# Performance work log

Hardware: AMD Instinct MI355X
Metric: run time of the kernel (lower is better)

## Reference

```python
import jax, jax.numpy as jnp
import numpy as np

B, S, D, H = 2, 2048, 2048, 16
DK = D // H  # 128


def _rope(x, cos, sin):
    # x: [B,S,H,DK]; pairs (x0,x1),(x2,x3),... rotated as complex numbers
    xr = x[..., 0::2]  # [B,S,H,DK/2]
    xi = x[..., 1::2]
    yr = xr * cos - xi * sin
    yi = xr * sin + xi * cos
    y = jnp.stack([yr, yi], axis=-1)  # [B,S,H,DK/2,2]
    return y.reshape(x.shape)


def setup_inputs() -> dict:
    key = jax.random.key(0)
    ks = jax.random.split(key, 12)
    sc = 1.0 / np.sqrt(D)
    q = jax.random.normal(ks[0], (B, S, D), jnp.float32)
    k = jax.random.normal(ks[1], (B, S, D), jnp.float32)
    v = jax.random.normal(ks[2], (B, S, D), jnp.float32)
    mask = jnp.tril(jnp.ones((S, S), jnp.int32))[None, None]  # causal [1,1,S,S]
    # standard RoPE angles: pos * theta^(-2i/dk)
    theta = 10000.0 ** (-jnp.arange(0, DK, 2, dtype=jnp.float32) / DK)  # [DK/2]
    freqs_angles = jnp.arange(S, dtype=jnp.float32)[:, None] * theta[None, :]  # [S,DK/2]
    wq = jax.random.normal(ks[3], (D, D), jnp.float32) * sc
    bq = jax.random.normal(ks[4], (D,), jnp.float32) * 0.01
    wk = jax.random.normal(ks[5], (D, D), jnp.float32) * sc
    bk = jax.random.normal(ks[6], (D,), jnp.float32) * 0.01
    wv = jax.random.normal(ks[7], (D, D), jnp.float32) * sc
    bv = jax.random.normal(ks[8], (D,), jnp.float32) * 0.01
    wo = jax.random.normal(ks[9], (D, D), jnp.float32) * sc
    bo = jax.random.normal(ks[10], (D,), jnp.float32) * 0.01
    return dict(q=q, k=k, v=v, mask=mask, freqs_angles=freqs_angles,
                wq=wq, bq=bq, wk=wk, bk=bk, wv=wv, bv=bv, wo=wo, bo=bo)


def reference(q, k, v, mask, freqs_angles, wq, bq, wk, bk, wv, bv, wo, bo):
    query = q @ wq.T + bq
    key_ = k @ wk.T + bk
    value = v @ wv.T + bv
    query = query.reshape(B, S, H, DK)
    key_ = key_.reshape(B, S, H, DK)
    value = value.reshape(B, S, H, DK).transpose(0, 2, 1, 3)  # [B,H,S,DK]
    cos = jnp.cos(freqs_angles)[None, :, None, :]  # [1,S,1,DK/2]
    sin = jnp.sin(freqs_angles)[None, :, None, :]
    query = _rope(query, cos, sin).transpose(0, 2, 1, 3)  # [B,H,S,DK]
    key_ = _rope(key_, cos, sin).transpose(0, 2, 1, 3)
    scores = jnp.einsum('bhqd,bhkd->bhqk', query, key_) / jnp.sqrt(jnp.float32(DK))
    scores = jnp.where(mask == 0, jnp.float32(-1e9), scores)
    attn = jax.nn.softmax(scores, axis=-1)  # dropout p=0.0 -> identity
    x = jnp.einsum('bhqk,bhkd->bhqd', attn, value)
    x = x.transpose(0, 2, 1, 3).reshape(B, S, D)
    return x @ wo.T + bo
```

## Files before the change

### kernel.cpp

```cpp
#include <hip/hip_runtime.h>
#include <hip/hip_bf16.h>

#define BB 2
#define SS 2048
#define DD 2048
#define HH 16
#define DKK 128
#define MM (BB*SS)

typedef unsigned short u16;
typedef short bf16x8 __attribute__((ext_vector_type(8)));
typedef unsigned short u16x8 __attribute__((ext_vector_type(8)));
typedef float f32x4 __attribute__((ext_vector_type(4)));

static __device__ __forceinline__ f32x4 mfma_bf16(bf16x8 a, bf16x8 b, f32x4 c) {
  return __builtin_amdgcn_mfma_f32_16x16x32_bf16(a, b, c, 0, 0, 0);
}

static __device__ __forceinline__ u16 f2b(float f) {
  unsigned int u = __float_as_uint(f);
  u = (u + 0x7FFFu + ((u >> 16) & 1u)) >> 16;
  return (u16)u;
}

static __device__ __forceinline__ u16 f2bq(float f) {
  unsigned int r;
  asm("v_cvt_pk_bf16_f32 %0, %1, %2" : "=v"(r) : "v"(f), "v"(f));
  return (u16)r;
}

static __device__ __forceinline__ void gl16(const u16* g, u16* l) {
  __builtin_amdgcn_global_load_lds(
      (const __attribute__((address_space(1))) unsigned int*)(const void*)g,
      (__attribute__((address_space(3))) unsigned int*)(void*)l, 16, 0, 0);
}

#define BARRIER() asm volatile("s_barrier" ::: "memory")

struct F2BArgs { const float* src[7]; u16* dst[7]; };
__global__ __launch_bounds__(256) void k_f2bf_all(F2BArgs a) {
  int bid = blockIdx.x;
  int buf, local;
  if (bid < 12288) { buf = bid >> 12; local = bid & 4095; }
  else { int t = bid - 12288; buf = 3 + (t >> 11); local = t & 2047; }
  const int i = (local * 256 + threadIdx.x) * 8;
  const float* in = a.src[buf];
  float4 v0 = *reinterpret_cast<const float4*>(in + i);
  float4 v1 = *reinterpret_cast<const float4*>(in + i + 4);
  u16x8 o;
  o[0]=f2b(v0.x); o[1]=f2b(v0.y); o[2]=f2b(v0.z); o[3]=f2b(v0.w);
  o[4]=f2b(v1.x); o[5]=f2b(v1.y); o[6]=f2b(v1.z); o[7]=f2b(v1.w);
  *reinterpret_cast<u16x8*>(a.dst[buf] + i) = o;
}

__global__ void k_cs(const float* __restrict__ fa, float* __restrict__ cs, int n) {
  int t = blockIdx.x * blockDim.x + threadIdx.x;
  if (t >= n) return;
  float a = fa[t];
  cs[2*t]   = cosf(a);
  cs[2*t+1] = sinf(a);
}

struct GemmJob { const u16* A; const u16* W; const float* bias; void* out; int mode; };
struct GemmArgs { GemmJob job[3]; };

__global__ __launch_bounds__(512, 2) void k_gemm256(GemmArgs ga, const float* __restrict__ cs) {
  const GemmJob J = ga.job[blockIdx.z];
  const u16* __restrict__ A = J.A;
  const u16* __restrict__ W = J.W;
  const int mode = J.mode;
  const int K = DD, N = DD;
  const int KT = K / 64;

  __shared__ __align__(16) u16 sA[2][256 * 64];
  __shared__ __align__(16) u16 sB[2][256 * 64];

  const int tid = threadIdx.x;
  const int l  = tid & 63;
  const int w  = tid >> 6;
  const int wm = w >> 2;
  const int wn = w & 3;
  const int bm = blockIdx.x * 256, bn = blockIdx.y * 256;
  const int lr = l & 15;
  const int lg = l >> 4;
  const int rx = (lr & 7) * 8;

  const int srcx = ((l & 7) * 8) ^ ((l >> 3) * 8);
  const size_t rowA = (size_t)(bm + w*16 + (l >> 3)) * K + srcx;
  const size_t rowB = (size_t)(bn + w*16 + (l >> 3)) * K + srcx;
  const int ldsrow = (w * 16) * 64;

  f32x4 acc[8][4];
#pragma unroll
  for (int m = 0; m < 8; m++)
#pragma unroll
    for (int n = 0; n < 4; n++)
#pragma unroll
      for (int j = 0; j < 4; j++) acc[m][n][j] = 0.0f;

  auto stA = [&](int kt, int h) {
    const u16* g = A + rowA + (size_t)h * 128 * K + kt * 64;
    u16* d = &sA[kt & 1][h * 128 * 64 + ldsrow];
    gl16(g, d);
    gl16(g + (size_t)8 * K, d + 8 * 64);
  };
  auto stB = [&](int kt, int h) {
    const u16* g = W + rowB + (size_t)h * 128 * K + kt * 64;
    u16* d = &sB[kt & 1][h * 128 * 64 + ldsrow];
    gl16(g, d);
    gl16(g + (size_t)8 * K, d + 8 * 64);
  };

  stB(0, 0); stB(0, 1); stA(0, 0); stA(0, 1);
  stB(1, 0); stB(1, 1);
  asm volatile("s_waitcnt vmcnt(4)" ::: "memory");
  BARRIER();

#pragma unroll 1
  for (int t = 0; t < KT; t++) {
    const u16* a_ = sA[t & 1];
    const u16* b_ = sB[t & 1];
    bf16x8 a03[4][2], a47[4][2], b01[2][2], b23[2][2];

#pragma unroll
    for (int m = 0; m < 4; m++)
#pragma unroll
      for (int kk = 0; kk < 2; kk++)
        a03[m][kk] = *reinterpret_cast<const bf16x8*>(
            a_ + (wm*128 + m*16 + lr) * 64 + ((kk*32 + lg*8) ^ rx));
#pragma unroll
    for (int n = 0; n < 2; n++)
#pragma unroll
      for (int kk = 0; kk < 2; kk++)
        b01[n][kk] = *reinterpret_cast<const bf16x8*>(
            b_ + (wn*64 + n*16 + lr) * 64 + ((kk*32 + lg*8) ^ rx));
    if (t + 1 < KT) stA(t + 1, 0);
    BARRIER();
    __builtin_amdgcn_s_setprio(1);
#pragma unroll
    for (int kk = 0; kk < 2; kk++)
#pragma unroll
      for (int m = 0; m < 4; m++)
#pragma unroll
        for (int n = 0; n < 2; n++)
          acc[m][n] = mfma_bf16(a03[m][kk], b01[n][kk], acc[m][n]);
    __builtin_amdgcn_s_setprio(0);
    BARRIER();

#pragma unroll
    for (int n = 0; n < 2; n++)
#pragma unroll
      for (int kk = 0; kk < 2; kk++)
        b23[n][kk] = *reinterpret_cast<const bf16x8*>(
            b_ + (wn*64 + (n + 2)*16 + lr) * 64 + ((kk*32 + lg*8) ^ rx));
    if (t + 1 < KT) stA(t + 1, 1);
    BARRIER();
    __builtin_amdgcn_s_setprio(1);
#pragma unroll
    for (int kk = 0; kk < 2; kk++)
#pragma unroll
      for (int m = 0; m < 4; m++)
#pragma unroll
        for (int n = 0; n < 2; n++)
          acc[m][n + 2] = mfma_bf16(a03[m][kk], b23[n][kk], acc[m][n + 2]);
    __builtin_amdgcn_s_setprio(0);
    BARRIER();

#pragma unroll
    for (int m = 0; m < 4; m++)
#pragma unroll
      for (int kk = 0; kk < 2; kk++)
        a47[m][kk] = *reinterpret_cast<const bf16x8*>(
            a_ + (wm*128 + (m + 4)*16 + lr) * 64 + ((kk*32 + lg*8) ^ rx));
    if (t + 2 < KT) stB(t + 2, 0);
    BARRIER();
    __builtin_amdgcn_s_setprio(1);
#pragma unroll
    for (int kk = 0; kk < 2; kk++)
#pragma unroll
      for (int m = 0; m < 4; m++)
#pragma unroll
        for (int n = 0; n < 2; n++)
          acc[m + 4][n] = mfma_bf16(a47[m][kk], b01[n][kk], acc[m + 4][n]);
    __builtin_amdgcn_s_setprio(0);
    BARRIER();

    if (t + 2 < KT) stB(t + 2, 1);
    BARRIER();
    __builtin_amdgcn_s_setprio(1);
#pragma unroll
    for (int kk = 0; kk < 2; kk++)
#pragma unroll
      for (int m = 0; m < 4; m++)
#pragma unroll
        for (int n = 0; n < 2; n++)
          acc[m + 4][n + 2] = mfma_bf16(a47[m][kk], b23[n][kk], acc[m + 4][n + 2]);
    __builtin_amdgcn_s_setprio(0);
    if (t + 2 < KT) {
      asm volatile("s_waitcnt vmcnt(4)" ::: "memory");
    } else {
      asm volatile("s_waitcnt vmcnt(0)" ::: "memory");
    }
    BARRIER();
  }

  float bv[4];
#pragma unroll
  for (int n = 0; n < 4; n++) bv[n] = J.bias[bn + wn*64 + n*16 + lr];
#pragma unroll
  for (int m = 0; m < 8; m++) {
#pragma unroll
    for (int n = 0; n < 4; n++) {
      const int col = bn + wn*64 + n*16 + lr;
#pragma unroll
      for (int r = 0; r < 4; r++) {
        const int row = bm + wm*128 + m*16 + lg*4 + r;
        float v = acc[m][n][r] + bv[n];
        if (mode & 1) {
          const int s  = row & (SS - 1);
          const int dk = col & (DKK - 1);
          const int p  = dk >> 1;
          const float2 csv = *reinterpret_cast<const float2*>(cs + (size_t)(s*64 + p)*2);
          const float other = __shfl_xor(v, 1);
          const float sgn = (dk & 1) ? csv.y : -csv.y;
          v = v * csv.x + other * sgn;
          if (mode == 3) v *= 0.12751744f;
        }
        if (mode == 2) {
          reinterpret_cast<float*>(J.out)[(size_t)row * N + col] = v;
        } else {
          reinterpret_cast<u16*>(J.out)[(size_t)row * N + col] = f2b(v);
        }
      }
    }
  }
}

__global__ __launch_bounds__(256) void k_gemm3(GemmArgs ga, const float* __restrict__ cs) {
  const GemmJob J = ga.job[blockIdx.z];
  const u16* __restrict__ A = J.A;
  const u16* __restrict__ W = J.W;
  const int mode = J.mode;
  const int K = DD, N = DD;

  __shared__ __align__(16) u16 sA[128 * 64];
  __shared__ __align__(16) u16 sB[128 * 64];
  const int tid = threadIdx.x;
  const int l  = tid & 63;
  const int w  = tid >> 6;
  const int wr = w >> 1, wc = w & 1;
  const int bm = blockIdx.x * 128, bn = blockIdx.y * 128;
  const int lr = l & 15;
  const int lg = l >> 4;

  f32x4 acc[4][4];
#pragma unroll
  for (int mi = 0; mi < 4; mi++)
#pragma unroll
    for (int ni = 0; ni < 4; ni++)
#pragma unroll
      for (int j = 0; j < 4; j++) acc[mi][ni][j] = 0.0f;

  const int srcx = ((l & 7) * 8) ^ ((l >> 3) * 8);
  const u16* gAl = A + (size_t)(bm + w*32 + (l >> 3)) * K + srcx;
  const u16* gBl = W + (size_t)(bn + w*32 + (l >> 3)) * K + srcx;

  const int rx = (lr & 7) * 8;

  for (int k0 = 0; k0 < K; k0 += 64) {
    __syncthreads();
#pragma unroll
    for (int i = 0; i < 4; i++) gl16(gAl + (size_t)i*8*K + k0, sA + (w*32 + i*8) * 64);
#pragma unroll
    for (int i = 0; i < 4; i++) gl16(gBl + (size_t)i*8*K + k0, sB + (w*32 + i*8) * 64);
    __syncthreads();

#pragma unroll
    for (int kk = 0; kk < 2; kk++) {
      bf16x8 af[4], bfv[4];
#pragma unroll
      for (int i = 0; i < 4; i++)
        af[i]  = *reinterpret_cast<const bf16x8*>(
            sA + (wr*64 + i*16 + lr) * 64 + ((kk*32 + lg*8) ^ rx));
#pragma unroll
      for (int i = 0; i < 4; i++)
        bfv[i] = *reinterpret_cast<const bf16x8*>(
            sB + (wc*64 + i*16 + lr) * 64 + ((kk*32 + lg*8) ^ rx));
#pragma unroll
      for (int mi = 0; mi < 4; mi++)
#pragma unroll
        for (int ni = 0; ni < 4; ni++)
          acc[mi][ni] = mfma_bf16(af[mi], bfv[ni], acc[mi][ni]);
    }
  }

#pragma unroll
  for (int mi = 0; mi < 4; mi++) {
#pragma unroll
    for (int ni = 0; ni < 4; ni++) {
      const int col = bn + wc*64 + ni*16 + lr;
      const float bv = J.bias[col];
#pragma unroll
      for (int r = 0; r < 4; r++) {
        const int row = bm + wr*64 + mi*16 + lg*4 + r;
        float v = acc[mi][ni][r] + bv;
        if (mode & 1) {
          const int s  = row & (SS - 1);
          const int dk = col & (DKK - 1);
          const int p  = dk >> 1;
          const float2 csv = *reinterpret_cast<const float2*>(cs + (size_t)(s*64 + p)*2);
          const float other = __shfl_xor(v, 1);
          const float sgn = (dk & 1) ? csv.y : -csv.y;
          v = v * csv.x + other * sgn;
          if (mode == 3) v *= 0.12751744f;
        }
        if (mode == 2) {
          reinterpret_cast<float*>(J.out)[(size_t)row * N + col] = v;
        } else {
          reinterpret_cast<u16*>(J.out)[(size_t)row * N + col] = f2b(v);
        }
      }
    }
  }
}

__global__ __launch_bounds__(256, 1) void k_attn(const u16* __restrict__ Qp,
                                                 const u16* __restrict__ Kp,
                                                 const u16* __restrict__ Vp,
                                                 u16* __restrict__ Op) {
  const int bid = blockIdx.x;
  const int qt = 15 - (bid >> 5);
  const int bh = bid & 31;
  const int h  = bh & 15;
  const int b  = bh >> 4;
  const int tid = threadIdx.x;
  const int l  = tid & 63, w = tid >> 6;
  const int lr = l & 15, lg = l >> 4;

  __shared__ __align__(16) u16 Klds[2 * 128 * 128];
  __shared__ __align__(16) u16 VT[128 * 128];
  __shared__ __align__(16) u16 PL[4][32][136];

  int koff[8];
#pragma unroll
  for (int i = 0; i < 8; i++) {
    const int row = w*32 + i*4 + (l >> 4);
    koff[i] = row * DD + (((l & 15) * 8) ^ ((row & 7) * 8));
  }
  const u16* kbase = Kp + (size_t)b * SS * DD + h * DKK;

  const int k0v = (tid >> 4) * 8;
  const int d0  = (tid & 15) * 8;
  const u16* vbase = Vp + (size_t)b * SS * DD + h * DKK + (size_t)k0v * DD + d0;

  uint4 vr[8];

  auto stageK = [&](int nk, int bufq) {
    const u16* kb = kbase + (size_t)nk * (128 * DD);
    u16* dst = Klds + bufq * 16384 + (w * 32) * 128;
#pragma unroll
    for (int i = 0; i < 8; i++) gl16(kb + koff[i], dst + i * 512);
  };
  auto prefV = [&](int nk) {
    const u16* vb = vbase + (size_t)nk * (128 * DD);
#pragma unroll
    for (int c = 0; c < 8; c++) vr[c] = *reinterpret_cast<const uint4*>(vb + c * DD);
  };

  int cur = 0;
  stageK(0, 0);
  prefV(0);

  bf16x8 qf[2][4];
#pragma unroll
  for (int mt = 0; mt < 2; mt++) {
    const size_t qrow = (size_t)(b*SS + qt*128 + w*32 + mt*16 + lr) * DD + h*DKK;
#pragma unroll
    for (int kk = 0; kk < 4; kk++)
      qf[mt][kk] = *reinterpret_cast<const bf16x8*>(Qp + qrow + kk*32 + lg*8);
  }

  float m[2][4], lsum[2][4];
  f32x4 oacc[2][8];
#pragma unroll
  for (int mt = 0; mt < 2; mt++)
#pragma unroll
    for (int r = 0; r < 4; r++) { m[mt][r] = -INFINITY; lsum[mt][r] = 0.0f; }
#pragma unroll
  for (int mt = 0; mt < 2; mt++)
#pragma unroll
    for (int dt = 0; dt < 8; dt++)
#pragma unroll
      for (int jj = 0; jj < 4; jj++) oacc[mt][dt][jj] = 0.0f;

#pragma unroll 1
  for (int kv = 0; kv <= qt; kv++) {
    __syncthreads();
#pragma unroll
    for (int dj = 0; dj < 8; dj++) {
      const int row = d0 + dj;
      const int col = k0v ^ (((row ^ (row >> 3)) & 15) * 8);
      u16x8 pk;
#pragma unroll
      for (int j = 0; j < 8; j++) pk[j] = reinterpret_cast<const u16*>(&vr[j])[dj];
      *reinterpret_cast<u16x8*>(VT + row * 128 + col) = pk;
    }
    __syncthreads();

    const bool hasnext = (kv < qt);
    if (hasnext) {
      prefV(kv + 1);
      stageK(kv + 1, cur ^ 1);
    }

    f32x4 sa[2][8];
#pragma unroll
    for (int mt = 0; mt < 2; mt++)
#pragma unroll
      for (int kt = 0; kt < 8; kt++)
#pragma unroll
        for (int jj = 0; jj < 4; jj++) sa[mt][kt][jj] = 0.0f;
    const u16* kl = Klds + cur * 16384;
    __builtin_amdgcn_s_setprio(1);
#pragma unroll
    for (int kk = 0; kk < 4; kk++) {
#pragma unroll
      for (int kt = 0; kt < 8; kt++) {
        const int row = kt*16 + lr;
        const bf16x8 kf = *reinterpret_cast<const bf16x8*>(
            kl + row * 128 + ((kk*32 + lg*8) ^ ((row & 7) * 8)));
#pragma unroll
        for (int mt = 0; mt < 2; mt++)
          sa[mt][kt] = mfma_bf16(qf[mt][kk], kf, sa[mt][kt]);
      }
    }
    __builtin_amdgcn_s_setprio(0);

    if (kv == qt) {
#pragma unroll
      for (int kt = 0; kt < 8; kt++) {
        const int key = kv*128 + kt*16 + lr;
#pragma unroll
        for (int mt = 0; mt < 2; mt++)
#pragma unroll
          for (int r = 0; r < 4; r++) {
            const int qv = qt*128 + w*32 + mt*16 + lg*4 + r;
            if (key > qv) sa[mt][kt][r] = -1e9f;
          }
      }
    }

    float pm[2][4];
#pragma unroll
    for (int mt = 0; mt < 2; mt++)
#pragma unroll
      for (int r = 0; r < 4; r++) {
        float t0 = fmaxf(fmaxf(sa[mt][0][r], sa[mt][1][r]), fmaxf(sa[mt][2][r], sa[mt][3][r]));
        float t1 = fmaxf(fmaxf(sa[mt][4][r], sa[mt][5][r]), fmaxf(sa[mt][6][r], sa[mt][7][r]));
        pm[mt][r] = fmaxf(t0, t1);
      }
    bool ok = true;
#pragma unroll
    for (int mt = 0; mt < 2; mt++)
#pragma unroll
      for (int r = 0; r < 4; r++) ok = ok && (pm[mt][r] <= m[mt][r] + 8.0f);
    if (!__all(ok)) {
#pragma unroll
      for (int mt = 0; mt < 2; mt++)
#pragma unroll
        for (int r = 0; r < 4; r++) {
          float t = pm[mt][r];
#pragma unroll
          for (int d = 1; d < 16; d <<= 1) t = fmaxf(t, __shfl_xor(t, d));
          const float mnew = fmaxf(m[mt][r], t);
          const float corr = exp2f(m[mt][r] - mnew);
          lsum[mt][r] *= corr;
#pragma unroll
          for (int dt = 0; dt < 8; dt++) oacc[mt][dt][r] *= corr;
          m[mt][r] = mnew;
        }
    }

#pragma unroll
    for (int mt = 0; mt < 2; mt++)
#pragma unroll
      for (int r = 0; r < 4; r++) {
        float rs = 0.0f;
#pragma unroll
        for (int kt = 0; kt < 8; kt++) {
          const float e = exp2f(sa[mt][kt][r] - m[mt][r]);
          rs += e;
          PL[w][mt*16 + lg*4 + r][kt*16 + lr] = f2bq(e);
        }
        lsum[mt][r] += rs;
      }

    __builtin_amdgcn_s_setprio(1);
#pragma unroll
    for (int kk2 = 0; kk2 < 4; kk2++) {
      bf16x8 pa[2];
#pragma unroll
      for (int mt = 0; mt < 2; mt++)
        pa[mt] = *reinterpret_cast<const bf16x8*>(&PL[w][mt*16 + lr][kk2*32 + lg*8]);
#pragma unroll
      for (int dt = 0; dt < 8; dt++) {
        const int row = dt*16 + lr;
        const bf16x8 vb = *reinterpret_cast<const bf16x8*>(
            VT + row * 128 + ((kk2*32 + lg*8) ^ (((row ^ (row >> 3)) & 15) * 8)));
#pragma unroll
        for (int mt = 0; mt < 2; mt++)
          oacc[mt][dt] = mfma_bf16(pa[mt], vb, oacc[mt][dt]);
      }
    }
    __builtin_amdgcn_s_setprio(0);

    if (hasnext) cur ^= 1;
  }

  float inv[2][4];
#pragma unroll
  for (int mt = 0; mt < 2; mt++)
#pragma unroll
    for (int r = 0; r < 4; r++) {
      float t = lsum[mt][r];
#pragma unroll
      for (int d = 1; d < 16; d <<= 1) t += __shfl_xor(t, d);
      inv[mt][r] = 1.0f / t;
    }
#pragma unroll
  for (int mt = 0; mt < 2; mt++)
#pragma unroll
    for (int dt = 0; dt < 8; dt++)
#pragma unroll
      for (int r = 0; r < 4; r++) {
        const size_t row = (size_t)(b*SS + qt*128 + w*32 + mt*16 + lg*4 + r);
        Op[row * DD + h*DKK + dt*16 + lr] = f2bq(oacc[mt][dt][r] * inv[mt][r]);
      }
}

extern "C" void kernel_launch(void* const* d_in, const int* in_sizes, int n_in,
                              void* d_out, int out_size, void* d_ws, size_t ws_size,
                              hipStream_t stream) {
  const float* q  = (const float*)d_in[0];
  const float* k  = (const float*)d_in[1];
  const float* v  = (const float*)d_in[2];
  const float* fa = (const float*)d_in[4];
  const float* wq = (const float*)d_in[5];
  const float* bq = (const float*)d_in[6];
  const float* wk = (const float*)d_in[7];
  const float* bk = (const float*)d_in[8];
  const float* wv = (const float*)d_in[9];
  const float* bv = (const float*)d_in[10];
  const float* wo = (const float*)d_in[11];
  const float* bo = (const float*)d_in[12];

  float* cs = (float*)d_ws;
  u16* bf = (u16*)((char*)d_ws + (size_t)262144 * sizeof(float));
  const size_t NX = (size_t)MM * DD;
  const size_t NW = (size_t)DD * DD;
  u16* q_bf  = bf;
  u16* k_bf  = q_bf + NX;
  u16* v_bf  = k_bf + NX;
  u16* wq_bf = v_bf + NX;
  u16* wk_bf = wq_bf + NW;
  u16* wv_bf = wk_bf + NW;
  u16* wo_bf = wv_bf + NW;
  u16* Qp    = wo_bf + NW;
  u16* Kp    = Qp + NX;
  u16* Vp    = Kp + NX;
  u16* Ao    = Vp + NX;

  F2BArgs fa7;
  fa7.src[0] = q;  fa7.dst[0] = q_bf;
  fa7.src[1] = k;  fa7.dst[1] = k_bf;
  fa7.src[2] = v;  fa7.dst[2] = v_bf;
  fa7.src[3] = wq; fa7.dst[3] = wq_bf;
  fa7.src[4] = wk; fa7.dst[4] = wk_bf;
  fa7.src[5] = wv; fa7.dst[5] = wv_bf;
  fa7.src[6] = wo; fa7.dst[6] = wo_bf;
  k_f2bf_all<<<dim3(20480), 256, 0, stream>>>(fa7);
  k_cs<<<dim3(131072/256), 256, 0, stream>>>(fa, cs, 131072);

  GemmArgs gq;
  gq.job[0] = GemmJob{ q_bf, wq_bf, bq, (void*)Qp, 3 };
  gq.job[1] = GemmJob{ k_bf, wk_bf, bk, (void*)Kp, 1 };
  gq.job[2] = GemmJob{ v_bf, wv_bf, bv, (void*)Vp, 0 };
  k_gemm256<<<dim3(MM/256, DD/256, 3), 512, 0, stream>>>(gq, cs);

  k_attn<<<dim3(512), 256, 0, stream>>>(Qp, Kp, Vp, Ao);

  GemmArgs go;
  go.job[0] = GemmJob{ Ao, wo_bf, bo, d_out, 2 };
  go.job[1] = go.job[0];
  go.job[2] = go.job[0];
  k_gemm3<<<dim3(MM/128, DD/128, 1), 256, 0, stream>>>(go, cs);
}
```

Measured before the change: 348.3 us.

## Reorder GEMM tile load quarters to prefetch A further ahead, pin schedule

```diff
diff --git a/kernel.cpp b/kernel.cpp
--- a/kernel.cpp
+++ b/kernel.cpp
@@ -86,9 +86,7 @@
   const int rx = (lr & 7) * 8;
 
   const int srcx = ((l & 7) * 8) ^ ((l >> 3) * 8);
-  const size_t rowA = (size_t)(bm + w*16 + (l >> 3)) * K + srcx;
-  const size_t rowB = (size_t)(bn + w*16 + (l >> 3)) * K + srcx;
-  const int ldsrow = (w * 16) * 64;
+  const int l3 = l >> 3;
 
   f32x4 acc[8][4];
 #pragma unroll
@@ -98,22 +96,24 @@
 #pragma unroll
       for (int j = 0; j < 4; j++) acc[m][n][j] = 0.0f;
 
-  auto stA = [&](int kt, int h) {
-    const u16* g = A + rowA + (size_t)h * 128 * K + kt * 64;
-    u16* d = &sA[kt & 1][h * 128 * 64 + ldsrow];
+  auto stA2 = [&](int kt, int q) {
+    const int R0 = (w & 3) * 16 + (w >> 2) * 128 + q * 64;
+    const u16* g = A + (size_t)(bm + R0 + l3) * K + srcx + kt * 64;
+    u16* d = &sA[kt & 1][R0 * 64];
     gl16(g, d);
     gl16(g + (size_t)8 * K, d + 8 * 64);
   };
-  auto stB = [&](int kt, int h) {
-    const u16* g = W + rowB + (size_t)h * 128 * K + kt * 64;
-    u16* d = &sB[kt & 1][h * 128 * 64 + ldsrow];
+  auto stB2 = [&](int kt, int q) {
+    const int R0 = (w >> 1) * 64 + (w & 1) * 16 + q * 32;
+    const u16* g = W + (size_t)(bn + R0 + l3) * K + srcx + kt * 64;
+    u16* d = &sB[kt & 1][R0 * 64];
     gl16(g, d);
     gl16(g + (size_t)8 * K, d + 8 * 64);
   };
 
-  stB(0, 0); stB(0, 1); stA(0, 0); stA(0, 1);
-  stB(1, 0); stB(1, 1);
-  asm volatile("s_waitcnt vmcnt(4)" ::: "memory");
+  stA2(0, 0); stA2(0, 1); stB2(0, 0); stB2(0, 1);
+  stA2(1, 0); stB2(1, 0); stB2(1, 1);
+  asm volatile("s_waitcnt vmcnt(6)" ::: "memory");
   BARRIER();
 
 #pragma unroll 1
@@ -134,8 +134,9 @@
       for (int kk = 0; kk < 2; kk++)
         b01[n][kk] = *reinterpret_cast<const bf16x8*>(
             b_ + (wn*64 + n*16 + lr) * 64 + ((kk*32 + lg*8) ^ rx));
-    if (t + 1 < KT) stA(t + 1, 0);
-    BARRIER();
+    if (t + 1 < KT) stA2(t + 1, 1);
+    BARRIER();
+    __builtin_amdgcn_sched_barrier(0);
     __builtin_amdgcn_s_setprio(1);
 #pragma unroll
     for (int kk = 0; kk < 2; kk++)
@@ -145,6 +146,7 @@
         for (int n = 0; n < 2; n++)
           acc[m][n] = mfma_bf16(a03[m][kk], b01[n][kk], acc[m][n]);
     __builtin_amdgcn_s_setprio(0);
+    __builtin_amdgcn_sched_barrier(0);
     BARRIER();
 
 #pragma unroll
@@ -153,8 +155,9 @@
       for (int kk = 0; kk < 2; kk++)
         b23[n][kk] = *reinterpret_cast<const bf16x8*>(
             b_ + (wn*64 + (n + 2)*16 + lr) * 64 + ((kk*32 + lg*8) ^ rx));
-    if (t + 1 < KT) stA(t + 1, 1);
-    BARRIER();
+    if (t + 2 < KT) stA2(t + 2, 0);
+    BARRIER();
+    __builtin_amdgcn_sched_barrier(0);
     __builtin_amdgcn_s_setprio(1);
 #pragma unroll
     for (int kk = 0; kk < 2; kk++)
@@ -164,6 +167,7 @@
         for (int n = 0; n < 2; n++)
           acc[m][n + 2] = mfma_bf16(a03[m][kk], b23[n][kk], acc[m][n + 2]);
     __builtin_amdgcn_s_setprio(0);
+    __builtin_amdgcn_sched_barrier(0);
     BARRIER();
 
 #pragma unroll
@@ -172,8 +176,9 @@
       for (int kk = 0; kk < 2; kk++)
         a47[m][kk] = *reinterpret_cast<const bf16x8*>(
             a_ + (wm*128 + (m + 4)*16 + lr) * 64 + ((kk*32 + lg*8) ^ rx));
-    if (t + 2 < KT) stB(t + 2, 0);
-    BARRIER();
+    if (t + 2 < KT) stB2(t + 2, 0);
+    BARRIER();
+    __builtin_amdgcn_sched_barrier(0);
     __builtin_amdgcn_s_setprio(1);
 #pragma unroll
     for (int kk = 0; kk < 2; kk++)
@@ -183,10 +188,12 @@
         for (int n = 0; n < 2; n++)
           acc[m + 4][n] = mfma_bf16(a47[m][kk], b01[n][kk], acc[m + 4][n]);
     __builtin_amdgcn_s_setprio(0);
-    BARRIER();
-
-    if (t + 2 < KT) stB(t + 2, 1);
-    BARRIER();
+    __builtin_amdgcn_sched_barrier(0);
+    BARRIER();
+
+    if (t + 2 < KT) stB2(t + 2, 1);
+    BARRIER();
+    __builtin_amdgcn_sched_barrier(0);
     __builtin_amdgcn_s_setprio(1);
 #pragma unroll
     for (int kk = 0; kk < 2; kk++)
@@ -196,8 +203,9 @@
         for (int n = 0; n < 2; n++)
           acc[m + 4][n + 2] = mfma_bf16(a47[m][kk], b23[n][kk], acc[m + 4][n + 2]);
     __builtin_amdgcn_s_setprio(0);
-    if (t + 2 < KT) {
-      asm volatile("s_waitcnt vmcnt(4)" ::: "memory");
+    __builtin_amdgcn_sched_barrier(0);
+    if (t < KT - 2) {
+      asm volatile("s_waitcnt vmcnt(6)" ::: "memory");
     } else {
       asm volatile("s_waitcnt vmcnt(0)" ::: "memory");
     }
```

Measured after the change: 345.2 us. About the same (-0.9%).
